# Kernel optimization log

Hardware: AMD Instinct MI355X
Metric: run time of the kernel (lower is better)

## Reference

```python
import jax, jax.numpy as jnp
import numpy as np

N = 100_000      # nodes
E = 3_200_000    # edges (avg degree 32)
F_IN = 64        # num_node_features
G = 256          # graphs in batch


def _lin(key, fan_in, fan_out):
    kw, kb = jax.random.split(key)
    bound = 1.0 / np.sqrt(fan_in)
    W = jax.random.uniform(kw, (fan_in, fan_out), jnp.float32, -bound, bound)
    b = jax.random.uniform(kb, (fan_out,), jnp.float32, -bound, bound)
    return W, b


def setup_inputs() -> dict:
    key = jax.random.key(0)
    ks = jax.random.split(key, 9)
    x = jax.random.normal(ks[0], (N, F_IN), jnp.float32)
    edge_index = jax.random.randint(ks[1], (2, E), 0, N, dtype=jnp.int64)
    batch = jnp.sort(jax.random.randint(ks[2], (N,), 0, G, dtype=jnp.int64))
    W1, b1 = _lin(ks[3], F_IN, 60)
    W2, b2 = _lin(ks[4], 60, 50)
    Wf1, bf1 = _lin(ks[5], 50, 30)
    Wf2, bf2 = _lin(ks[6], 30, 20)
    Wf3, bf3 = _lin(ks[7], 20, 10)
    Wo, bo = _lin(ks[8], 10, 1)
    return {"x": x, "edge_index": edge_index, "batch": batch,
            "W1": W1, "b1": b1, "W2": W2, "b2": b2,
            "Wf1": Wf1, "bf1": bf1, "Wf2": Wf2, "bf2": bf2,
            "Wf3": Wf3, "bf3": bf3, "Wo": Wo, "bo": bo}


def _gcn_norm(edge_index, n_nodes):
    # add self loops, then symmetric D^{-1/2} (A+I) D^{-1/2} edge weights
    loop = jnp.arange(n_nodes, dtype=edge_index.dtype)
    src = jnp.concatenate([edge_index[0], loop])
    dst = jnp.concatenate([edge_index[1], loop])
    deg = jax.ops.segment_sum(jnp.ones_like(dst, dtype=jnp.float32), dst,
                              num_segments=n_nodes)
    dinv = jax.lax.rsqrt(deg)  # deg >= 1 thanks to self loops
    norm = dinv[src] * dinv[dst]
    return src, dst, norm


def _gcn_conv(h, W, b, src, dst, norm, n_nodes):
    h = h @ W                                            # [N, out]
    msg = h[src] * norm[:, None]                         # gather over edges
    agg = jax.ops.segment_sum(msg, dst, num_segments=n_nodes)
    return agg + b


def reference(x, edge_index, batch, W1, b1, W2, b2,
              Wf1, bf1, Wf2, bf2, Wf3, bf3, Wo, bo):
    n_nodes = x.shape[0]
    src, dst, norm = _gcn_norm(edge_index, n_nodes)
    h = _gcn_conv(x, W1, b1, src, dst, norm, n_nodes)    # [N, 60]
    h = _gcn_conv(h, W2, b2, src, dst, norm, n_nodes)    # [N, 50]
    # global_add_pool over graph ids
    g = jax.ops.segment_sum(h, batch, num_segments=G)    # [G, 50]
    # MLP stack (no nonlinearities in the original forward)
    g = g @ Wf1 + bf1
    g = g @ Wf2 + bf2
    g = g @ Wf3 + bf3
    return g @ Wo + bo                                   # [G, 1]
```

## Files before the change

### kernel.cpp

```cpp
#include <hip/hip_runtime.h>


#define RSHIFT 7
#define RNODES 128
#define NB_MAX 1024
#define STHREADS 512
#define CTHREADS 1024
#define STAGE_CAP 8192
#define BCAP 6144

#define LOAD_QUAD(ii, cc, P0, P1, P2, P3, B0, B1, B2, B3, R0, R1, R2, R3)     \
    if (cc == 4) {                                                            \
        int4 s4 = *reinterpret_cast<const int4*>(src + ii);                   \
        int4 d4 = *reinterpret_cast<const int4*>(dst + ii);                   \
        P0 = (unsigned)s4.x | ((unsigned)(d4.x & (RNODES-1)) << 17);          \
        P1 = (unsigned)s4.y | ((unsigned)(d4.y & (RNODES-1)) << 17);          \
        P2 = (unsigned)s4.z | ((unsigned)(d4.z & (RNODES-1)) << 17);          \
        P3 = (unsigned)s4.w | ((unsigned)(d4.w & (RNODES-1)) << 17);          \
        B0 = d4.x >> RSHIFT; B1 = d4.y >> RSHIFT;                             \
        B2 = d4.z >> RSHIFT; B3 = d4.w >> RSHIFT;                             \
        R0 = atomicAdd(&hist[B0], 1);                                         \
        R1 = atomicAdd(&hist[B1], 1);                                         \
        R2 = atomicAdd(&hist[B2], 1);                                         \
        R3 = atomicAdd(&hist[B3], 1);                                         \
    } else {                                                                  \
        if (cc > 0) { int s=src[ii],   d=dst[ii];   P0=(unsigned)s|((unsigned)(d&(RNODES-1))<<17); B0=d>>RSHIFT; R0=atomicAdd(&hist[B0],1); } \
        if (cc > 1) { int s=src[ii+1], d=dst[ii+1]; P1=(unsigned)s|((unsigned)(d&(RNODES-1))<<17); B1=d>>RSHIFT; R1=atomicAdd(&hist[B1],1); } \
        if (cc > 2) { int s=src[ii+2], d=dst[ii+2]; P2=(unsigned)s|((unsigned)(d&(RNODES-1))<<17); B2=d>>RSHIFT; R2=atomicAdd(&hist[B2],1); } \
    }

#define STOREG_QUAD(cc, P0, P1, P2, P3, B0, B1, B2, B3, R0, R1, R2, R3)       \
    if (cc > 0) binned[(size_t)B0 * BCAP + lbase[B0] + R0] = P0;              \
    if (cc > 1) binned[(size_t)B1 * BCAP + lbase[B1] + R1] = P1;              \
    if (cc > 2) binned[(size_t)B2 * BCAP + lbase[B2] + R2] = P2;              \
    if (cc > 3) binned[(size_t)B3 * BCAP + lbase[B3] + R3] = P3;

__global__ __launch_bounds__(STHREADS, 4)
void scatter_k(const float* __restrict__ x,
               const int* __restrict__ src, const int* __restrict__ dst,
               const float* __restrict__ W1, const float* __restrict__ b1,
               const float* __restrict__ W2, const float* __restrict__ b2,
               const float* __restrict__ Wf1, const float* __restrict__ bf1,
               const float* __restrict__ Wf2, const float* __restrict__ bf2,
               const float* __restrict__ Wf3, const float* __restrict__ bf3,
               const float* __restrict__ Wo, const float* __restrict__ bo,
               float* __restrict__ u, float* __restrict__ scG,
               int E, int n, int npb, int nb,
               int* __restrict__ cursor, unsigned int* __restrict__ binned) {
    __shared__ int hist[NB_MAX];
    __shared__ int lbase[NB_MAX];
    __shared__ float wtmp[224];
    __shared__ float w1c_s[64];
    const int tid = threadIdx.x;
    const int bx = blockIdx.x;

    {
        float* wo  = wtmp;
        float* w3  = wtmp + 16;
        float* w2  = wtmp + 48;
        float* w1  = wtmp + 80;
        float* w2c = wtmp + 144;
        hist[tid] = 0; hist[tid + STHREADS] = 0;
        if (tid < 10) wo[tid] = Wo[tid];
        __syncthreads();
        if (tid < 20) { float s = 0.f; for (int j = 0; j < 10; ++j) s += Wf3[tid*10+j]*wo[j]; w3[tid] = s; }
        __syncthreads();
        if (tid < 30) { float s = 0.f; for (int j = 0; j < 20; ++j) s += Wf2[tid*20+j]*w3[j]; w2[tid] = s; }
        __syncthreads();
        if (tid < 50) { float s = 0.f; for (int j = 0; j < 30; ++j) s += Wf1[tid*30+j]*w2[j]; w1[tid] = s; }
        __syncthreads();
        if (tid < 60) { float s = 0.f; for (int j = 0; j < 50; ++j) s += W2[tid*50+j]*w1[j]; w2c[tid] = s; }
        __syncthreads();
        if (tid < 64) { float s = 0.f; for (int j = 0; j < 60; ++j) s += W1[tid*60+j]*w2c[j]; w1c_s[tid] = s; }
        if (bx == 0 && tid == 0) {
            float c1 = 0.f; for (int j = 0; j < 60; ++j) c1 += b1[j]*w2c[j];
            float c2 = 0.f; for (int j = 0; j < 50; ++j) c2 += b2[j]*w1[j];
            float c0 = bo[0];
            for (int j = 0; j < 30; ++j) c0 += bf1[j]*w2[j];
            for (int j = 0; j < 20; ++j) c0 += bf2[j]*w3[j];
            for (int j = 0; j < 10; ++j) c0 += bf3[j]*wo[j];
            scG[0] = c1; scG[1] = c2; scG[2] = c0;
        }
        __syncthreads();
    }

    {
        const int grp = tid >> 4, sub = tid & 15;
        float4 wv = *reinterpret_cast<const float4*>(&w1c_s[sub * 4]);
        int base = bx * npb;
        for (int p = 0; p * 32 < npb; ++p) {
            int nl = p * 32 + grp;
            int g = base + nl;
            bool ok = (nl < npb) && (g < n);
            float val = 0.f;
            if (ok) {
                float4 xv = *reinterpret_cast<const float4*>(
                    x + (size_t)g * 64 + sub * 4);
                val = xv.x*wv.x + xv.y*wv.y + xv.z*wv.z + xv.w*wv.w;
            }
            val += __shfl_down(val, 8, 16);
            val += __shfl_down(val, 4, 16);
            val += __shfl_down(val, 2, 16);
            val += __shfl_down(val, 1, 16);
            if (ok && sub == 0) u[g] = val;
        }
    }

    int e0 = bx * STAGE_CAP;
    int e1 = e0 + STAGE_CAP; if (e1 > E) e1 = E;

    unsigned pa0=0,pa1=0,pa2=0,pa3=0, pb0=0,pb1=0,pb2=0,pb3=0;
    unsigned pc0=0,pc1=0,pc2=0,pc3=0, pd0=0,pd1=0,pd2=0,pd3=0;
    int ba0=0,ba1=0,ba2=0,ba3=0, bb0=0,bb1=0,bb2=0,bb3=0;
    int bc0=0,bc1=0,bc2=0,bc3=0, bd0=0,bd1=0,bd2=0,bd3=0;
    int ra0=0,ra1=0,ra2=0,ra3=0, rb0=0,rb1=0,rb2=0,rb3=0;
    int rc0=0,rc1=0,rc2=0,rc3=0, rd0=0,rd1=0,rd2=0,rd3=0;

    int iA = e0 + tid * 4;
    int iB = iA + STHREADS * 4;
    int iC = iB + STHREADS * 4;
    int iD = iC + STHREADS * 4;
    int cA = e1 - iA; if (cA > 4) cA = 4; if (cA < 0) cA = 0;
    int cB = e1 - iB; if (cB > 4) cB = 4; if (cB < 0) cB = 0;
    int cC = e1 - iC; if (cC > 4) cC = 4; if (cC < 0) cC = 0;
    int cD = e1 - iD; if (cD > 4) cD = 4; if (cD < 0) cD = 0;

    LOAD_QUAD(iA, cA, pa0,pa1,pa2,pa3, ba0,ba1,ba2,ba3, ra0,ra1,ra2,ra3)
    LOAD_QUAD(iB, cB, pb0,pb1,pb2,pb3, bb0,bb1,bb2,bb3, rb0,rb1,rb2,rb3)
    LOAD_QUAD(iC, cC, pc0,pc1,pc2,pc3, bc0,bc1,bc2,bc3, rc0,rc1,rc2,rc3)
    LOAD_QUAD(iD, cD, pd0,pd1,pd2,pd3, bd0,bd1,bd2,bd3, rd0,rd1,rd2,rd3)
    __syncthreads();

    {
        int b0 = tid, b1 = tid + STHREADS;
        int h0 = hist[b0], h1 = hist[b1];
        if (h0 > 0) lbase[b0] = atomicAdd(&cursor[b0], h0);
        if (h1 > 0) lbase[b1] = atomicAdd(&cursor[b1], h1);
    }
    __syncthreads();

    STOREG_QUAD(cA, pa0,pa1,pa2,pa3, ba0,ba1,ba2,ba3, ra0,ra1,ra2,ra3)
    STOREG_QUAD(cB, pb0,pb1,pb2,pb3, bb0,bb1,bb2,bb3, rb0,rb1,rb2,rb3)
    STOREG_QUAD(cC, pc0,pc1,pc2,pc3, bc0,bc1,bc2,bc3, rc0,rc1,rc2,rc3)
    STOREG_QUAD(cD, pd0,pd1,pd2,pd3, bd0,bd1,bd2,bd3, rd0,rd1,rd2,rd3)
}

__global__ __launch_bounds__(CTHREADS, 2)
void sort_dinv_k(unsigned int* __restrict__ binned,
                 const int* __restrict__ cursor,
                 const float* __restrict__ u,
                 float* __restrict__ dinv, float* __restrict__ w,
                 int* __restrict__ offG, int n) {
    __shared__ unsigned eIn[BCAP];
    __shared__ unsigned eOut[BCAP];
    __shared__ int cnt[RNODES];
    __shared__ int off[RNODES];
    __shared__ int pos[RNODES];
    const int tid = threadIdx.x, b = blockIdx.x;
    if (tid < RNODES) cnt[tid] = 0;
    __syncthreads();
    size_t s0 = (size_t)b * BCAP;
    int c = cursor[b];
    if (c > BCAP) c = BCAP;
    int nvec = c >> 2;
    for (int k = tid; k < nvec; k += CTHREADS) {
        uint4 p = *reinterpret_cast<const uint4*>(binned + s0 + 4 * (size_t)k);
        eIn[4*k+0] = p.x; eIn[4*k+1] = p.y; eIn[4*k+2] = p.z; eIn[4*k+3] = p.w;
        atomicAdd(&cnt[p.x >> 17], 1);
        atomicAdd(&cnt[p.y >> 17], 1);
        atomicAdd(&cnt[p.z >> 17], 1);
        atomicAdd(&cnt[p.w >> 17], 1);
    }
    for (int i = 4 * nvec + tid; i < c; i += CTHREADS) {
        unsigned p = binned[s0 + i];
        eIn[i] = p;
        atomicAdd(&cnt[p >> 17], 1);
    }
    __syncthreads();
    int hval = (tid < RNODES) ? cnt[tid] : 0;
    if (tid < RNODES) off[tid] = hval;
    __syncthreads();
    for (int o = 1; o < RNODES; o <<= 1) {
        int a = 0;
        if (tid < RNODES && tid >= o) a = off[tid - o];
        __syncthreads();
        if (tid < RNODES) off[tid] += a;
        __syncthreads();
    }
    if (tid < RNODES) {
        int e = off[tid] - hval;
        off[tid] = e;
        pos[tid] = e;
    }
    __syncthreads();
    for (int i = tid; i < c; i += CTHREADS) {
        unsigned p = eIn[i];
        int r = atomicAdd(&pos[p >> 17], 1);
        eOut[r] = p;
    }
    __syncthreads();
    for (int k = tid; k < nvec; k += CTHREADS) {
        uint4 p;
        p.x = eOut[4*k+0]; p.y = eOut[4*k+1]; p.z = eOut[4*k+2]; p.w = eOut[4*k+3];
        *reinterpret_cast<uint4*>(binned + s0 + 4 * (size_t)k) = p;
    }
    for (int i = 4 * nvec + tid; i < c; i += CTHREADS)
        binned[s0 + i] = eOut[i];
    if (tid < RNODES) {
        int g = (b << RSHIFT) + tid;
        if (g < n) {
            float d = rsqrtf((float)(cnt[tid] + 1));
            dinv[g] = d;
            w[g] = d * u[g];
            offG[g] = off[tid];
        }
    }
}

__global__ __launch_bounds__(CTHREADS, 2)
void conv_mid_k(const unsigned int* __restrict__ binned,
                const int* __restrict__ cursor, const int* __restrict__ offG,
                const float* __restrict__ w, const float* __restrict__ dinv,
                const float* __restrict__ u, const float* __restrict__ sc,
                float* __restrict__ v, float* __restrict__ wb,
                float* __restrict__ out, int n, int G) {
    __shared__ int off_s[RNODES + 1];
    int tid = threadIdx.x, b = blockIdx.x;
    if (b == 0 && tid < G) out[tid] = sc[2];
    size_t s0 = (size_t)b * BCAP;
    int c = cursor[b];
    if (c > BCAP) c = BCAP;
    if (tid < RNODES) {
        int g = (b << RSHIFT) + tid;
        off_s[tid] = (g < n) ? offG[g] : c;
    }
    if (tid == 0) off_s[RNODES] = c;
    __syncthreads();
    int node = tid >> 3, sub = tid & 7;
    int g = (b << RSHIFT) + node;
    int o0 = off_s[node], o1 = off_s[node + 1];
    float s = 0.f;
    for (int k = o0 + sub; k < o1; k += 8) {
        unsigned p = binned[s0 + k];
        s += w[p & 0x1FFFF];
    }
    s += __shfl_xor(s, 1, 8);
    s += __shfl_xor(s, 2, 8);
    s += __shfl_xor(s, 4, 8);
    if (sub == 0 && g < n) {
        float di = dinv[g];
        float val = sc[0] + di * s + di * di * u[g];
        v[g] = val;
        wb[g] = di * val;
    }
}

__global__ __launch_bounds__(CTHREADS, 2)
void conv_final_k(const unsigned int* __restrict__ binned,
                  const int* __restrict__ cursor, const int* __restrict__ offG,
                  const float* __restrict__ wbv, const float* __restrict__ dinv,
                  const float* __restrict__ v, const float* __restrict__ sc,
                  const int* __restrict__ batch, float* __restrict__ out, int n) {
    __shared__ int off_s[RNODES + 1];
    __shared__ float tbuf[RNODES];
    __shared__ int gbuf[RNODES];
    int tid = threadIdx.x, b = blockIdx.x;
    size_t s0 = (size_t)b * BCAP;
    int c = cursor[b];
    if (c > BCAP) c = BCAP;
    if (tid < RNODES) {
        int g = (b << RSHIFT) + tid;
        off_s[tid] = (g < n) ? offG[g] : c;
    }
    if (tid == 0) off_s[RNODES] = c;
    __syncthreads();
    int node = tid >> 3, sub = tid & 7;
    int g = (b << RSHIFT) + node;
    int o0 = off_s[node], o1 = off_s[node + 1];
    float s = 0.f;
    for (int k = o0 + sub; k < o1; k += 8) {
        unsigned p = binned[s0 + k];
        s += wbv[p & 0x1FFFF];
    }
    s += __shfl_xor(s, 1, 8);
    s += __shfl_xor(s, 2, 8);
    s += __shfl_xor(s, 4, 8);
    if (sub == 0) {
        float tval = 0.f; int gid = -1;
        if (g < n) {
            float di = dinv[g];
            tval = sc[1] + di * s + di * di * v[g];
            gid = batch[g];
        }
        tbuf[node] = tval;
        gbuf[node] = gid;
    }
    __syncthreads();
    if (tid < RNODES) {
        int g2 = (b << RSHIFT) + tid;
        if (g2 < n) {
            int gid = gbuf[tid];
            bool head = (tid == 0) || (gbuf[tid - 1] != gid);
            if (head) {
                float sum = 0.f;
                int i2 = tid;
                while (i2 < RNODES && gbuf[i2] == gid) { sum += tbuf[i2]; ++i2; }
                atomicAdd(&out[gid], sum);
            }
        }
    }
}

extern "C" void kernel_launch(void* const* d_in, const int* in_sizes, int n_in,
                              void* d_out, int out_size, void* d_ws, size_t ws_size,
                              hipStream_t stream)
{
    const float* x    = (const float*)d_in[0];
    const int*   ei   = (const int*)d_in[1];
    const int*   batch= (const int*)d_in[2];
    const float* W1   = (const float*)d_in[3];
    const float* b1   = (const float*)d_in[4];
    const float* W2   = (const float*)d_in[5];
    const float* b2   = (const float*)d_in[6];
    const float* Wf1  = (const float*)d_in[7];
    const float* bf1  = (const float*)d_in[8];
    const float* Wf2  = (const float*)d_in[9];
    const float* bf2  = (const float*)d_in[10];
    const float* Wf3  = (const float*)d_in[11];
    const float* bf3  = (const float*)d_in[12];
    const float* Wo   = (const float*)d_in[13];
    const float* bo   = (const float*)d_in[14];
    float* out = (float*)d_out;

    const int n = in_sizes[0] / 64;
    const int E = in_sizes[1] / 2;
    const int G = out_size;
    const int* src = ei;
    const int* dst = ei + E;
    const int nb = (n + RNODES - 1) >> RSHIFT;

    float* ws_f = (float*)d_ws;
    int*   ws_i = (int*)d_ws;
    int*   cursor = ws_i;
    float* scG    = ws_f + NB_MAX;
    size_t off_u  = NB_MAX + 16;
    float* u      = ws_f + off_u;
    float* dinv   = u + n;
    float* w      = dinv + n;
    float* v      = w + n;
    float* wb     = v + n;
    int*   offG   = ws_i + off_u + 5*(size_t)n;
    size_t off_b  = off_u + 6*(size_t)n;
    off_b = (off_b + 3) & ~(size_t)3;
    unsigned int* binned = (unsigned int*)(ws_f + off_b);

    const int NT = (E + STAGE_CAP - 1) / STAGE_CAP;
    const int npb = (n + NT - 1) / NT;

    hipMemsetAsync(cursor, 0, NB_MAX * sizeof(int), stream);
    hipLaunchKernelGGL(scatter_k, dim3(NT), dim3(STHREADS), 0, stream,
                       x, src, dst,
                       W1, b1, W2, b2, Wf1, bf1, Wf2, bf2, Wf3, bf3, Wo, bo,
                       u, scG, E, n, npb, nb, cursor, binned);
    hipLaunchKernelGGL(sort_dinv_k, dim3(nb), dim3(CTHREADS), 0, stream,
                       binned, cursor, u, dinv, w, offG, n);
    hipLaunchKernelGGL(conv_mid_k, dim3(nb), dim3(CTHREADS), 0, stream,
                       binned, cursor, offG, w, dinv, u, scG, v, wb, out, n, G);
    hipLaunchKernelGGL(conv_final_k, dim3(nb), dim3(CTHREADS), 0, stream,
                       binned, cursor, offG, wb, dinv, v, scG, batch, out, n);
}
```

Measured before the change: 204.7 us.

## Replace per-bin sort with split-bin shared-atomic accumulation and elementwise finalize kernels

Drops the in-shared-memory counting sort of each destination bin and the CSR offset-based segmented reductions. Each bin is now processed by two blocks that accumulate degree and weighted neighbor sums with shared-memory atomics, then flush them to global arrays with global atomics. Separate elementwise kernels compute dinv, the middle layer and the final pooled output. The scatter stage uses smaller edge tiles with more blocks and one quad per thread. This removes the sort's shared-memory traffic but adds extra kernel launches, global atomics and more global round trips, and the float atomics make the summation order nondeterministic.

After: 252.4 us. 1.23x slower.

```diff
diff --git a/kernel.cpp b/kernel.cpp
--- a/kernel.cpp
+++ b/kernel.cpp
@@ -5,35 +5,9 @@
 #define RNODES 128
 #define NB_MAX 1024
 #define STHREADS 512
-#define CTHREADS 1024
-#define STAGE_CAP 8192
+#define CTHREADS 512
+#define TILE_E 2048
 #define BCAP 6144
-
-#define LOAD_QUAD(ii, cc, P0, P1, P2, P3, B0, B1, B2, B3, R0, R1, R2, R3)     \
-    if (cc == 4) {                                                            \
-        int4 s4 = *reinterpret_cast<const int4*>(src + ii);                   \
-        int4 d4 = *reinterpret_cast<const int4*>(dst + ii);                   \
-        P0 = (unsigned)s4.x | ((unsigned)(d4.x & (RNODES-1)) << 17);          \
-        P1 = (unsigned)s4.y | ((unsigned)(d4.y & (RNODES-1)) << 17);          \
-        P2 = (unsigned)s4.z | ((unsigned)(d4.z & (RNODES-1)) << 17);          \
-        P3 = (unsigned)s4.w | ((unsigned)(d4.w & (RNODES-1)) << 17);          \
-        B0 = d4.x >> RSHIFT; B1 = d4.y >> RSHIFT;                             \
-        B2 = d4.z >> RSHIFT; B3 = d4.w >> RSHIFT;                             \
-        R0 = atomicAdd(&hist[B0], 1);                                         \
-        R1 = atomicAdd(&hist[B1], 1);                                         \
-        R2 = atomicAdd(&hist[B2], 1);                                         \
-        R3 = atomicAdd(&hist[B3], 1);                                         \
-    } else {                                                                  \
-        if (cc > 0) { int s=src[ii],   d=dst[ii];   P0=(unsigned)s|((unsigned)(d&(RNODES-1))<<17); B0=d>>RSHIFT; R0=atomicAdd(&hist[B0],1); } \
-        if (cc > 1) { int s=src[ii+1], d=dst[ii+1]; P1=(unsigned)s|((unsigned)(d&(RNODES-1))<<17); B1=d>>RSHIFT; R1=atomicAdd(&hist[B1],1); } \
-        if (cc > 2) { int s=src[ii+2], d=dst[ii+2]; P2=(unsigned)s|((unsigned)(d&(RNODES-1))<<17); B2=d>>RSHIFT; R2=atomicAdd(&hist[B2],1); } \
-    }
-
-#define STOREG_QUAD(cc, P0, P1, P2, P3, B0, B1, B2, B3, R0, R1, R2, R3)       \
-    if (cc > 0) binned[(size_t)B0 * BCAP + lbase[B0] + R0] = P0;              \
-    if (cc > 1) binned[(size_t)B1 * BCAP + lbase[B1] + R1] = P1;              \
-    if (cc > 2) binned[(size_t)B2 * BCAP + lbase[B2] + R2] = P2;              \
-    if (cc > 3) binned[(size_t)B3 * BCAP + lbase[B3] + R3] = P3;
 
 __global__ __launch_bounds__(STHREADS, 4)
 void scatter_k(const float* __restrict__ x,
@@ -45,6 +19,8 @@
                const float* __restrict__ Wf3, const float* __restrict__ bf3,
                const float* __restrict__ Wo, const float* __restrict__ bo,
                float* __restrict__ u, float* __restrict__ scG,
+               int* __restrict__ degG, float* __restrict__ accG,
+               float* __restrict__ acc2G,
                int E, int n, int npb, int nb,
                int* __restrict__ cursor, unsigned int* __restrict__ binned) {
     __shared__ int hist[NB_MAX];
@@ -85,9 +61,13 @@
     }
 
     {
+        int base = bx * npb;
+        for (int i = tid; i < npb; i += STHREADS) {
+            int g = base + i;
+            if (g < n) { degG[g] = 0; accG[g] = 0.f; acc2G[g] = 0.f; }
+        }
         const int grp = tid >> 4, sub = tid & 15;
         float4 wv = *reinterpret_cast<const float4*>(&w1c_s[sub * 4]);
-        int base = bx * npb;
         for (int p = 0; p * 32 < npb; ++p) {
             int nl = p * 32 + grp;
             int g = base + nl;
@@ -106,31 +86,33 @@
         }
     }
 
-    int e0 = bx * STAGE_CAP;
-    int e1 = e0 + STAGE_CAP; if (e1 > E) e1 = E;
-
-    unsigned pa0=0,pa1=0,pa2=0,pa3=0, pb0=0,pb1=0,pb2=0,pb3=0;
-    unsigned pc0=0,pc1=0,pc2=0,pc3=0, pd0=0,pd1=0,pd2=0,pd3=0;
-    int ba0=0,ba1=0,ba2=0,ba3=0, bb0=0,bb1=0,bb2=0,bb3=0;
-    int bc0=0,bc1=0,bc2=0,bc3=0, bd0=0,bd1=0,bd2=0,bd3=0;
-    int ra0=0,ra1=0,ra2=0,ra3=0, rb0=0,rb1=0,rb2=0,rb3=0;
-    int rc0=0,rc1=0,rc2=0,rc3=0, rd0=0,rd1=0,rd2=0,rd3=0;
-
+    int e0 = bx * TILE_E;
+    int e1 = e0 + TILE_E; if (e1 > E) e1 = E;
     int iA = e0 + tid * 4;
-    int iB = iA + STHREADS * 4;
-    int iC = iB + STHREADS * 4;
-    int iD = iC + STHREADS * 4;
     int cA = e1 - iA; if (cA > 4) cA = 4; if (cA < 0) cA = 0;
-    int cB = e1 - iB; if (cB > 4) cB = 4; if (cB < 0) cB = 0;
-    int cC = e1 - iC; if (cC > 4) cC = 4; if (cC < 0) cC = 0;
-    int cD = e1 - iD; if (cD > 4) cD = 4; if (cD < 0) cD = 0;
-
-    LOAD_QUAD(iA, cA, pa0,pa1,pa2,pa3, ba0,ba1,ba2,ba3, ra0,ra1,ra2,ra3)
-    LOAD_QUAD(iB, cB, pb0,pb1,pb2,pb3, bb0,bb1,bb2,bb3, rb0,rb1,rb2,rb3)
-    LOAD_QUAD(iC, cC, pc0,pc1,pc2,pc3, bc0,bc1,bc2,bc3, rc0,rc1,rc2,rc3)
-    LOAD_QUAD(iD, cD, pd0,pd1,pd2,pd3, bd0,bd1,bd2,bd3, rd0,rd1,rd2,rd3)
-    __syncthreads();
-
+
+    unsigned pk0=0,pk1=0,pk2=0,pk3=0;
+    int bk0=0,bk1=0,bk2=0,bk3=0;
+    int rk0=0,rk1=0,rk2=0,rk3=0;
+    if (cA == 4) {
+        int4 s4 = *reinterpret_cast<const int4*>(src + iA);
+        int4 d4 = *reinterpret_cast<const int4*>(dst + iA);
+        pk0 = (unsigned)s4.x | ((unsigned)(d4.x & (RNODES-1)) << 17);
+        pk1 = (unsigned)s4.y | ((unsigned)(d4.y & (RNODES-1)) << 17);
+        pk2 = (unsigned)s4.z | ((unsigned)(d4.z & (RNODES-1)) << 17);
+        pk3 = (unsigned)s4.w | ((unsigned)(d4.w & (RNODES-1)) << 17);
+        bk0 = d4.x >> RSHIFT; bk1 = d4.y >> RSHIFT;
+        bk2 = d4.z >> RSHIFT; bk3 = d4.w >> RSHIFT;
+        rk0 = atomicAdd(&hist[bk0], 1);
+        rk1 = atomicAdd(&hist[bk1], 1);
+        rk2 = atomicAdd(&hist[bk2], 1);
+        rk3 = atomicAdd(&hist[bk3], 1);
+    } else {
+        if (cA > 0) { int s=src[iA],   d=dst[iA];   pk0=(unsigned)s|((unsigned)(d&(RNODES-1))<<17); bk0=d>>RSHIFT; rk0=atomicAdd(&hist[bk0],1); }
+        if (cA > 1) { int s=src[iA+1], d=dst[iA+1]; pk1=(unsigned)s|((unsigned)(d&(RNODES-1))<<17); bk1=d>>RSHIFT; rk1=atomicAdd(&hist[bk1],1); }
+        if (cA > 2) { int s=src[iA+2], d=dst[iA+2]; pk2=(unsigned)s|((unsigned)(d&(RNODES-1))<<17); bk2=d>>RSHIFT; rk2=atomicAdd(&hist[bk2],1); }
+    }
+    __syncthreads();
     {
         int b0 = tid, b1 = tid + STHREADS;
         int h0 = hist[b0], h1 = hist[b1];
@@ -138,175 +120,169 @@
         if (h1 > 0) lbase[b1] = atomicAdd(&cursor[b1], h1);
     }
     __syncthreads();
-
-    STOREG_QUAD(cA, pa0,pa1,pa2,pa3, ba0,ba1,ba2,ba3, ra0,ra1,ra2,ra3)
-    STOREG_QUAD(cB, pb0,pb1,pb2,pb3, bb0,bb1,bb2,bb3, rb0,rb1,rb2,rb3)
-    STOREG_QUAD(cC, pc0,pc1,pc2,pc3, bc0,bc1,bc2,bc3, rc0,rc1,rc2,rc3)
-    STOREG_QUAD(cD, pd0,pd1,pd2,pd3, bd0,bd1,bd2,bd3, rd0,rd1,rd2,rd3)
-}
-
-__global__ __launch_bounds__(CTHREADS, 2)
-void sort_dinv_k(unsigned int* __restrict__ binned,
-                 const int* __restrict__ cursor,
-                 const float* __restrict__ u,
-                 float* __restrict__ dinv, float* __restrict__ w,
-                 int* __restrict__ offG, int n) {
-    __shared__ unsigned eIn[BCAP];
-    __shared__ unsigned eOut[BCAP];
+    if (cA > 0) binned[(size_t)bk0 * BCAP + lbase[bk0] + rk0] = pk0;
+    if (cA > 1) binned[(size_t)bk1 * BCAP + lbase[bk1] + rk1] = pk1;
+    if (cA > 2) binned[(size_t)bk2 * BCAP + lbase[bk2] + rk2] = pk2;
+    if (cA > 3) binned[(size_t)bk3 * BCAP + lbase[bk3] + rk3] = pk3;
+}
+
+__global__ __launch_bounds__(CTHREADS, 8)
+void degpart_k(const unsigned int* __restrict__ binned,
+               const int* __restrict__ cursor,
+               int* __restrict__ degG, int n) {
     __shared__ int cnt[RNODES];
-    __shared__ int off[RNODES];
-    __shared__ int pos[RNODES];
-    const int tid = threadIdx.x, b = blockIdx.x;
+    const int tid = threadIdx.x;
+    const int b = blockIdx.x >> 1, h = blockIdx.x & 1;
     if (tid < RNODES) cnt[tid] = 0;
     __syncthreads();
     size_t s0 = (size_t)b * BCAP;
     int c = cursor[b];
     if (c > BCAP) c = BCAP;
-    int nvec = c >> 2;
-    for (int k = tid; k < nvec; k += CTHREADS) {
-        uint4 p = *reinterpret_cast<const uint4*>(binned + s0 + 4 * (size_t)k);
-        eIn[4*k+0] = p.x; eIn[4*k+1] = p.y; eIn[4*k+2] = p.z; eIn[4*k+3] = p.w;
+    int mid = ((c >> 1) + 3) & ~3; if (mid > c) mid = c;
+    int lo = h ? mid : 0, hi = h ? c : mid;
+    int len = hi - lo, nq = len >> 2;
+    for (int k = tid; k < nq; k += CTHREADS) {
+        uint4 p = *reinterpret_cast<const uint4*>(binned + s0 + lo + 4 * (size_t)k);
         atomicAdd(&cnt[p.x >> 17], 1);
         atomicAdd(&cnt[p.y >> 17], 1);
         atomicAdd(&cnt[p.z >> 17], 1);
         atomicAdd(&cnt[p.w >> 17], 1);
     }
-    for (int i = 4 * nvec + tid; i < c; i += CTHREADS) {
-        unsigned p = binned[s0 + i];
-        eIn[i] = p;
-        atomicAdd(&cnt[p >> 17], 1);
-    }
-    __syncthreads();
-    int hval = (tid < RNODES) ? cnt[tid] : 0;
-    if (tid < RNODES) off[tid] = hval;
-    __syncthreads();
-    for (int o = 1; o < RNODES; o <<= 1) {
-        int a = 0;
-        if (tid < RNODES && tid >= o) a = off[tid - o];
-        __syncthreads();
-        if (tid < RNODES) off[tid] += a;
-        __syncthreads();
-    }
-    if (tid < RNODES) {
-        int e = off[tid] - hval;
-        off[tid] = e;
-        pos[tid] = e;
-    }
-    __syncthreads();
-    for (int i = tid; i < c; i += CTHREADS) {
-        unsigned p = eIn[i];
-        int r = atomicAdd(&pos[p >> 17], 1);
-        eOut[r] = p;
-    }
-    __syncthreads();
-    for (int k = tid; k < nvec; k += CTHREADS) {
-        uint4 p;
-        p.x = eOut[4*k+0]; p.y = eOut[4*k+1]; p.z = eOut[4*k+2]; p.w = eOut[4*k+3];
-        *reinterpret_cast<uint4*>(binned + s0 + 4 * (size_t)k) = p;
-    }
-    for (int i = 4 * nvec + tid; i < c; i += CTHREADS)
-        binned[s0 + i] = eOut[i];
+    for (int i = lo + 4 * nq + tid; i < hi; i += CTHREADS)
+        atomicAdd(&cnt[binned[s0 + i] >> 17], 1);
+    __syncthreads();
     if (tid < RNODES) {
         int g = (b << RSHIFT) + tid;
-        if (g < n) {
-            float d = rsqrtf((float)(cnt[tid] + 1));
-            dinv[g] = d;
-            w[g] = d * u[g];
-            offG[g] = off[tid];
-        }
-    }
-}
-
-__global__ __launch_bounds__(CTHREADS, 2)
-void conv_mid_k(const unsigned int* __restrict__ binned,
-                const int* __restrict__ cursor, const int* __restrict__ offG,
-                const float* __restrict__ w, const float* __restrict__ dinv,
-                const float* __restrict__ u, const float* __restrict__ sc,
-                float* __restrict__ v, float* __restrict__ wb,
-                float* __restrict__ out, int n, int G) {
-    __shared__ int off_s[RNODES + 1];
-    int tid = threadIdx.x, b = blockIdx.x;
-    if (b == 0 && tid < G) out[tid] = sc[2];
+        if (g < n && cnt[tid] != 0) atomicAdd(&degG[g], cnt[tid]);
+    }
+}
+
+__global__ __launch_bounds__(CTHREADS, 8)
+void finA_k(const int* __restrict__ degG, const float* __restrict__ u,
+            const float* __restrict__ scG,
+            float* __restrict__ dinv, float* __restrict__ w,
+            float* __restrict__ out, int n, int G) {
+    int g = blockIdx.x * CTHREADS + threadIdx.x;
+    if (blockIdx.x == 0 && threadIdx.x < G) out[threadIdx.x] = scG[2];
+    if (g < n) {
+        float d = rsqrtf((float)(degG[g] + 1));
+        dinv[g] = d;
+        w[g] = d * u[g];
+    }
+}
+
+__global__ __launch_bounds__(CTHREADS, 8)
+void midpart_k(const unsigned int* __restrict__ binned,
+               const int* __restrict__ cursor,
+               const float* __restrict__ w,
+               float* __restrict__ accG, int n) {
+    __shared__ float acc[RNODES];
+    const int tid = threadIdx.x;
+    const int b = blockIdx.x >> 1, h = blockIdx.x & 1;
+    if (tid < RNODES) acc[tid] = 0.f;
+    __syncthreads();
     size_t s0 = (size_t)b * BCAP;
     int c = cursor[b];
     if (c > BCAP) c = BCAP;
+    int mid = ((c >> 1) + 3) & ~3; if (mid > c) mid = c;
+    int lo = h ? mid : 0, hi = h ? c : mid;
+    int len = hi - lo, nq = len >> 2;
+    for (int k = tid; k < nq; k += CTHREADS) {
+        uint4 p = *reinterpret_cast<const uint4*>(binned + s0 + lo + 4 * (size_t)k);
+        float w0 = w[p.x & 0x1FFFF];
+        float w1 = w[p.y & 0x1FFFF];
+        float w2 = w[p.z & 0x1FFFF];
+        float w3 = w[p.w & 0x1FFFF];
+        atomicAdd(&acc[p.x >> 17], w0);
+        atomicAdd(&acc[p.y >> 17], w1);
+        atomicAdd(&acc[p.z >> 17], w2);
+        atomicAdd(&acc[p.w >> 17], w3);
+    }
+    for (int i = lo + 4 * nq + tid; i < hi; i += CTHREADS) {
+        unsigned p = binned[s0 + i];
+        atomicAdd(&acc[p >> 17], w[p & 0x1FFFF]);
+    }
+    __syncthreads();
     if (tid < RNODES) {
         int g = (b << RSHIFT) + tid;
-        off_s[tid] = (g < n) ? offG[g] : c;
-    }
-    if (tid == 0) off_s[RNODES] = c;
-    __syncthreads();
-    int node = tid >> 3, sub = tid & 7;
-    int g = (b << RSHIFT) + node;
-    int o0 = off_s[node], o1 = off_s[node + 1];
-    float s = 0.f;
-    for (int k = o0 + sub; k < o1; k += 8) {
-        unsigned p = binned[s0 + k];
-        s += w[p & 0x1FFFF];
-    }
-    s += __shfl_xor(s, 1, 8);
-    s += __shfl_xor(s, 2, 8);
-    s += __shfl_xor(s, 4, 8);
-    if (sub == 0 && g < n) {
-        float di = dinv[g];
-        float val = sc[0] + di * s + di * di * u[g];
+        if (g < n && acc[tid] != 0.f) atomicAdd(&accG[g], acc[tid]);
+    }
+}
+
+__global__ __launch_bounds__(CTHREADS, 8)
+void finB_k(const float* __restrict__ accG, const float* __restrict__ dinv,
+            const float* __restrict__ u, const float* __restrict__ scG,
+            float* __restrict__ v, float* __restrict__ wb, int n) {
+    int g = blockIdx.x * CTHREADS + threadIdx.x;
+    if (g < n) {
+        float d = dinv[g];
+        float val = scG[0] + d * accG[g] + d * d * u[g];
         v[g] = val;
-        wb[g] = di * val;
-    }
-}
-
-__global__ __launch_bounds__(CTHREADS, 2)
-void conv_final_k(const unsigned int* __restrict__ binned,
-                  const int* __restrict__ cursor, const int* __restrict__ offG,
-                  const float* __restrict__ wbv, const float* __restrict__ dinv,
-                  const float* __restrict__ v, const float* __restrict__ sc,
-                  const int* __restrict__ batch, float* __restrict__ out, int n) {
-    __shared__ int off_s[RNODES + 1];
-    __shared__ float tbuf[RNODES];
-    __shared__ int gbuf[RNODES];
-    int tid = threadIdx.x, b = blockIdx.x;
+        wb[g] = d * val;
+    }
+}
+
+__global__ __launch_bounds__(CTHREADS, 8)
+void finalpart_k(const unsigned int* __restrict__ binned,
+                 const int* __restrict__ cursor,
+                 const float* __restrict__ wbv,
+                 float* __restrict__ acc2G, int n) {
+    __shared__ float acc[RNODES];
+    const int tid = threadIdx.x;
+    const int b = blockIdx.x >> 1, h = blockIdx.x & 1;
+    if (tid < RNODES) acc[tid] = 0.f;
+    __syncthreads();
     size_t s0 = (size_t)b * BCAP;
     int c = cursor[b];
     if (c > BCAP) c = BCAP;
+    int mid = ((c >> 1) + 3) & ~3; if (mid > c) mid = c;
+    int lo = h ? mid : 0, hi = h ? c : mid;
+    int len = hi - lo, nq = len >> 2;
+    for (int k = tid; k < nq; k += CTHREADS) {
+        uint4 p = *reinterpret_cast<const uint4*>(binned + s0 + lo + 4 * (size_t)k);
+        float w0 = wbv[p.x & 0x1FFFF];
+        float w1 = wbv[p.y & 0x1FFFF];
+        float w2 = wbv[p.z & 0x1FFFF];
+        float w3 = wbv[p.w & 0x1FFFF];
+        atomicAdd(&acc[p.x >> 17], w0);
+        atomicAdd(&acc[p.y >> 17], w1);
+        atomicAdd(&acc[p.z >> 17], w2);
+        atomicAdd(&acc[p.w >> 17], w3);
+    }
+    for (int i = lo + 4 * nq + tid; i < hi; i += CTHREADS) {
+        unsigned p = binned[s0 + i];
+        atomicAdd(&acc[p >> 17], wbv[p & 0x1FFFF]);
+    }
+    __syncthreads();
     if (tid < RNODES) {
         int g = (b << RSHIFT) + tid;
-        off_s[tid] = (g < n) ? offG[g] : c;
-    }
-    if (tid == 0) off_s[RNODES] = c;
-    __syncthreads();
-    int node = tid >> 3, sub = tid & 7;
-    int g = (b << RSHIFT) + node;
-    int o0 = off_s[node], o1 = off_s[node + 1];
-    float s = 0.f;
-    for (int k = o0 + sub; k < o1; k += 8) {
-        unsigned p = binned[s0 + k];
-        s += wbv[p & 0x1FFFF];
-    }
-    s += __shfl_xor(s, 1, 8);
-    s += __shfl_xor(s, 2, 8);
-    s += __shfl_xor(s, 4, 8);
-    if (sub == 0) {
-        float tval = 0.f; int gid = -1;
-        if (g < n) {
-            float di = dinv[g];
-            tval = sc[1] + di * s + di * di * v[g];
-            gid = batch[g];
-        }
-        tbuf[node] = tval;
-        gbuf[node] = gid;
-    }
-    __syncthreads();
-    if (tid < RNODES) {
-        int g2 = (b << RSHIFT) + tid;
-        if (g2 < n) {
-            int gid = gbuf[tid];
-            bool head = (tid == 0) || (gbuf[tid - 1] != gid);
-            if (head) {
-                float sum = 0.f;
-                int i2 = tid;
-                while (i2 < RNODES && gbuf[i2] == gid) { sum += tbuf[i2]; ++i2; }
-                atomicAdd(&out[gid], sum);
-            }
+        if (g < n && acc[tid] != 0.f) atomicAdd(&acc2G[g], acc[tid]);
+    }
+}
+
+__global__ __launch_bounds__(CTHREADS, 8)
+void finC_k(const float* __restrict__ acc2G, const float* __restrict__ dinv,
+            const float* __restrict__ v, const float* __restrict__ scG,
+            const int* __restrict__ batch, float* __restrict__ out, int n) {
+    __shared__ float tbuf[CTHREADS];
+    __shared__ int gbuf[CTHREADS];
+    int tid = threadIdx.x;
+    int g = blockIdx.x * CTHREADS + tid;
+    float tval = 0.f; int gid = -1;
+    if (g < n) {
+        float d = dinv[g];
+        tval = scG[1] + d * acc2G[g] + d * d * v[g];
+        gid = batch[g];
+    }
+    tbuf[tid] = tval; gbuf[tid] = gid;
+    __syncthreads();
+    if (g < n) {
+        bool head = (tid == 0) || (gbuf[tid - 1] != gid);
+        if (head) {
+            float s = 0.f;
+            int i2 = tid;
+            while (i2 < CTHREADS && gbuf[i2] == gid) { s += tbuf[i2]; ++i2; }
+            atomicAdd(&out[gid], s);
         }
     }
 }
@@ -349,23 +325,32 @@
     float* w      = dinv + n;
     float* v      = w + n;
     float* wb     = v + n;
-    int*   offG   = ws_i + off_u + 5*(size_t)n;
-    size_t off_b  = off_u + 6*(size_t)n;
+    int*   degG   = ws_i + off_u + 5*(size_t)n;
+    float* accG   = ws_f + off_u + 6*(size_t)n;
+    float* acc2G  = accG + n;
+    size_t off_b  = off_u + 8*(size_t)n;
     off_b = (off_b + 3) & ~(size_t)3;
     unsigned int* binned = (unsigned int*)(ws_f + off_b);
 
-    const int NT = (E + STAGE_CAP - 1) / STAGE_CAP;
+    const int NT = (E + TILE_E - 1) / TILE_E;
     const int npb = (n + NT - 1) / NT;
+    const int NN = (n + CTHREADS - 1) / CTHREADS;
 
     hipMemsetAsync(cursor, 0, NB_MAX * sizeof(int), stream);
     hipLaunchKernelGGL(scatter_k, dim3(NT), dim3(STHREADS), 0, stream,
                        x, src, dst,
                        W1, b1, W2, b2, Wf1, bf1, Wf2, bf2, Wf3, bf3, Wo, bo,
-                       u, scG, E, n, npb, nb, cursor, binned);
-    hipLaunchKernelGGL(sort_dinv_k, dim3(nb), dim3(CTHREADS), 0, stream,
-                       binned, cursor, u, dinv, w, offG, n);
-    hipLaunchKernelGGL(conv_mid_k, dim3(nb), dim3(CTHREADS), 0, stream,
-                       binned, cursor, offG, w, dinv, u, scG, v, wb, out, n, G);
-    hipLaunchKernelGGL(conv_final_k, dim3(nb), dim3(CTHREADS), 0, stream,
-                       binned, cursor, offG, wb, dinv, v, scG, batch, out, n);
-}
+                       u, scG, degG, accG, acc2G, E, n, npb, nb, cursor, binned);
+    hipLaunchKernelGGL(degpart_k, dim3(2 * nb), dim3(CTHREADS), 0, stream,
+                       binned, cursor, degG, n);
+    hipLaunchKernelGGL(finA_k, dim3(NN), dim3(CTHREADS), 0, stream,
+                       degG, u, scG, dinv, w, out, n, G);
+    hipLaunchKernelGGL(midpart_k, dim3(2 * nb), dim3(CTHREADS), 0, stream,
+                       binned, cursor, w, accG, n);
+    hipLaunchKernelGGL(finB_k, dim3(NN), dim3(CTHREADS), 0, stream,
+                       accG, dinv, u, scG, v, wb, n);
+    hipLaunchKernelGGL(finalpart_k, dim3(2 * nb), dim3(CTHREADS), 0, stream,
+                       binned, cursor, wb, acc2G, n);
+    hipLaunchKernelGGL(finC_k, dim3(NN), dim3(CTHREADS), 0, stream,
+                       acc2G, dinv, v, scG, batch, out, n);
+}
```

## Stage binned edges in LDS via block-local prefix scan before coalesced global write

Applied to the files above, without the earlier changes.

The scatter kernel now runs a block-wide prefix scan over its per-bin histogram so each tile's edges can be placed contiguously by bin in shared memory. It then writes them to the global binned array with a linear thread-strided loop, so consecutive threads write adjacent addresses within each bin run. This replaces the old per-element scattered global stores and aims for better write coalescing. The cost is a 9-step scan with barriers, about 56KB of extra shared memory that may lower occupancy, and an extra LDS round trip.

Measured after the change: 198.1 us, median of 2. 3.2% less time.

```diff
diff --git a/kernel.cpp b/kernel.cpp
--- a/kernel.cpp
+++ b/kernel.cpp
@@ -29,11 +29,11 @@
         if (cc > 2) { int s=src[ii+2], d=dst[ii+2]; P2=(unsigned)s|((unsigned)(d&(RNODES-1))<<17); B2=d>>RSHIFT; R2=atomicAdd(&hist[B2],1); } \
     }
 
-#define STOREG_QUAD(cc, P0, P1, P2, P3, B0, B1, B2, B3, R0, R1, R2, R3)       \
-    if (cc > 0) binned[(size_t)B0 * BCAP + lbase[B0] + R0] = P0;              \
-    if (cc > 1) binned[(size_t)B1 * BCAP + lbase[B1] + R1] = P1;              \
-    if (cc > 2) binned[(size_t)B2 * BCAP + lbase[B2] + R2] = P2;              \
-    if (cc > 3) binned[(size_t)B3 * BCAP + lbase[B3] + R3] = P3;
+#define STORE_QUAD(cc, P0, P1, P2, P3, B0, B1, B2, B3, R0, R1, R2, R3)        \
+    if (cc > 0) { int s2 = tbase[B0] + R0; staged[s2] = P0; bof[s2] = (unsigned short)B0; } \
+    if (cc > 1) { int s2 = tbase[B1] + R1; staged[s2] = P1; bof[s2] = (unsigned short)B1; } \
+    if (cc > 2) { int s2 = tbase[B2] + R2; staged[s2] = P2; bof[s2] = (unsigned short)B2; } \
+    if (cc > 3) { int s2 = tbase[B3] + R3; staged[s2] = P3; bof[s2] = (unsigned short)B3; }
 
 __global__ __launch_bounds__(STHREADS, 4)
 void scatter_k(const float* __restrict__ x,
@@ -48,7 +48,11 @@
                int E, int n, int npb, int nb,
                int* __restrict__ cursor, unsigned int* __restrict__ binned) {
     __shared__ int hist[NB_MAX];
-    __shared__ int lbase[NB_MAX];
+    __shared__ int tbase[NB_MAX];
+    __shared__ int adj[NB_MAX];
+    __shared__ int sums[STHREADS];
+    __shared__ unsigned int staged[STAGE_CAP];
+    __shared__ unsigned short bof[STAGE_CAP];
     __shared__ float wtmp[224];
     __shared__ float w1c_s[64];
     const int tid = threadIdx.x;
@@ -131,18 +135,43 @@
     LOAD_QUAD(iD, cD, pd0,pd1,pd2,pd3, bd0,bd1,bd2,bd3, rd0,rd1,rd2,rd3)
     __syncthreads();
 
+    int h0 = hist[2*tid], h1 = hist[2*tid+1];
+    int pair = h0 + h1;
+    sums[tid] = pair;
+    __syncthreads();
+    for (int off = 1; off < STHREADS; off <<= 1) {
+        int a = (tid >= off) ? sums[tid - off] : 0;
+        __syncthreads();
+        sums[tid] += a;
+        __syncthreads();
+    }
+    int excl = sums[tid] - pair;
+    tbase[2*tid] = excl;
+    tbase[2*tid+1] = excl + h0;
     {
-        int b0 = tid, b1 = tid + STHREADS;
-        int h0 = hist[b0], h1 = hist[b1];
-        if (h0 > 0) lbase[b0] = atomicAdd(&cursor[b0], h0);
-        if (h1 > 0) lbase[b1] = atomicAdd(&cursor[b1], h1);
-    }
-    __syncthreads();
-
-    STOREG_QUAD(cA, pa0,pa1,pa2,pa3, ba0,ba1,ba2,ba3, ra0,ra1,ra2,ra3)
-    STOREG_QUAD(cB, pb0,pb1,pb2,pb3, bb0,bb1,bb2,bb3, rb0,rb1,rb2,rb3)
-    STOREG_QUAD(cC, pc0,pc1,pc2,pc3, bc0,bc1,bc2,bc3, rc0,rc1,rc2,rc3)
-    STOREG_QUAD(cD, pd0,pd1,pd2,pd3, bd0,bd1,bd2,bd3, rd0,rd1,rd2,rd3)
+        int b0 = 2*tid, b1 = 2*tid + 1;
+        if (b0 < nb && h0 > 0) {
+            int r = atomicAdd(&cursor[b0], h0);
+            adj[b0] = b0 * BCAP + r - excl;
+        }
+        if (b1 < nb && h1 > 0) {
+            int r = atomicAdd(&cursor[b1], h1);
+            adj[b1] = b1 * BCAP + r - (excl + h0);
+        }
+    }
+    __syncthreads();
+
+    STORE_QUAD(cA, pa0,pa1,pa2,pa3, ba0,ba1,ba2,ba3, ra0,ra1,ra2,ra3)
+    STORE_QUAD(cB, pb0,pb1,pb2,pb3, bb0,bb1,bb2,bb3, rb0,rb1,rb2,rb3)
+    STORE_QUAD(cC, pc0,pc1,pc2,pc3, bc0,bc1,bc2,bc3, rc0,rc1,rc2,rc3)
+    STORE_QUAD(cD, pd0,pd1,pd2,pd3, bd0,bd1,bd2,bd3, rd0,rd1,rd2,rd3)
+    __syncthreads();
+
+    int tcount = e1 - e0;
+    for (int s2 = tid; s2 < tcount; s2 += STHREADS) {
+        int b = bof[s2];
+        binned[adj[b] + s2] = staged[s2];
+    }
 }
 
 __global__ __launch_bounds__(CTHREADS, 2)
```
